# Performance work log

Measured on AMD Instinct MI355X. Metric: run time of the kernel, lower is better.

Reference implementation:

```python
import jax, jax.numpy as jnp
import numpy as np

N_NODES = 100000
N_EDGES = 500000
NODE_DIM = 32


def setup_inputs() -> dict:
    key = jax.random.key(0)
    k1, k2, k3, k4 = jax.random.split(key, 4)
    node_states = jax.random.normal(k1, (N_NODES, NODE_DIM), dtype=jnp.float32)
    edge_index = jax.random.randint(k2, (N_EDGES, 2), 0, N_NODES, dtype=jnp.int64)
    # Pre-encoded per-edge transform matrices (a_in), scaled like a learned encoder output
    a_in = jax.random.normal(k3, (N_EDGES, NODE_DIM, NODE_DIM), dtype=jnp.float32) / np.sqrt(NODE_DIM)
    bound = 1.0 / np.sqrt(NODE_DIM)
    bias = jax.random.uniform(k4, (NODE_DIM,), dtype=jnp.float32, minval=-bound, maxval=bound)
    return {"node_states": node_states, "edge_index": edge_index, "a_in": a_in, "bias": bias}


def reference(node_states, edge_index, a_in, bias):
    num_nodes, node_dim = node_states.shape
    src = edge_index[:, 0]  # message sender
    dst = edge_index[:, 1]  # message receiver
    # gather: [E, D]
    x_i = jnp.take(node_states, src, axis=0)
    # per-edge matmul: x_i[e] @ a_in[e] -> [E, D]
    msg = jnp.einsum('ed,edf->ef', x_i, a_in)
    # scatter-mean into node slots
    summed = jax.ops.segment_sum(msg, dst, num_segments=num_nodes)
    count = jax.ops.segment_sum(jnp.ones((msg.shape[0],), msg.dtype), dst, num_segments=num_nodes)
    mean = summed / jnp.maximum(count, 1.0)[:, None]
    return jax.nn.relu(mean + bias)
```

## Files before the change

kernel.cpp:

```cpp
#include <hip/hip_runtime.h>

#define NUM_NODES 100000
#define NODE_DIM 32

__global__ void mp_zero_kernel(float4* __restrict__ out4,
                               float4* __restrict__ cnt4,
                               int n_out4, int n_cnt4) {
    int t = blockIdx.x * blockDim.x + threadIdx.x;
    if (t < n_out4) {
        out4[t] = make_float4(0.f, 0.f, 0.f, 0.f);
    }
    int u = t - n_out4;
    if (u >= 0 && u < n_cnt4) {
        cnt4[u] = make_float4(0.f, 0.f, 0.f, 0.f);
    }
}

__global__ void mp_edge_kernel(const float* __restrict__ node_states,
                               const int* __restrict__ edge_index,
                               const float4* __restrict__ a4,
                               float* __restrict__ out_sum,
                               float* __restrict__ counts,
                               int n_edges) {
    int t = blockIdx.x * blockDim.x + threadIdx.x;
    int e = t >> 3;
    if (e >= n_edges) return;
    int j = t & 7;

    int src = edge_index[2 * e];
    int dst = edge_index[2 * e + 1];

    float4 x4 = reinterpret_cast<const float4*>(node_states)[src * 8 + j];
    float xs[4] = {x4.x, x4.y, x4.z, x4.w};

    const float4* A = a4 + (size_t)e * 256;
    float4 acc = make_float4(0.f, 0.f, 0.f, 0.f);

#pragma unroll
    for (int d = 0; d < 32; ++d) {
        float xd = __shfl(xs[d & 3], d >> 2, 8);
        float4 a = A[d * 8 + j];
        acc.x = fmaf(xd, a.x, acc.x);
        acc.y = fmaf(xd, a.y, acc.y);
        acc.z = fmaf(xd, a.z, acc.z);
        acc.w = fmaf(xd, a.w, acc.w);
    }

    float* o = out_sum + (size_t)dst * NODE_DIM + j * 4;
    atomicAdd(o + 0, acc.x);
    atomicAdd(o + 1, acc.y);
    atomicAdd(o + 2, acc.z);
    atomicAdd(o + 3, acc.w);
    if (j == 0) atomicAdd(counts + dst, 1.0f);
}

__global__ void mp_finalize_kernel(float4* __restrict__ out4,
                                   const float* __restrict__ counts,
                                   const float4* __restrict__ bias4,
                                   int n_nodes) {
    int t = blockIdx.x * blockDim.x + threadIdx.x;
    if (t >= n_nodes * 8) return;
    int n = t >> 3;
    int j = t & 7;
    float c = fmaxf(counts[n], 1.0f);
    float inv = 1.0f / c;
    float4 s = out4[t];
    float4 b = bias4[j];
    float4 r;
    r.x = fmaxf(fmaf(s.x, inv, b.x), 0.f);
    r.y = fmaxf(fmaf(s.y, inv, b.y), 0.f);
    r.z = fmaxf(fmaf(s.z, inv, b.z), 0.f);
    r.w = fmaxf(fmaf(s.w, inv, b.w), 0.f);
    out4[t] = r;
}

extern "C" void kernel_launch(void* const* d_in, const int* in_sizes, int n_in,
                              void* d_out, int out_size, void* d_ws, size_t ws_size,
                              hipStream_t stream) {
    const float* node_states = (const float*)d_in[0];
    const int*   edge_index  = (const int*)d_in[1];
    const float* a_in        = (const float*)d_in[2];
    const float* bias        = (const float*)d_in[3];

    int n_edges = in_sizes[1] / 2;
    int n_nodes = in_sizes[0] / NODE_DIM;

    float* out_sum = (float*)d_out;
    float* counts  = (float*)d_ws;

    int n_out4 = n_nodes * (NODE_DIM / 4);
    int n_cnt4 = (n_nodes + 3) / 4;
    {
        int total = n_out4 + n_cnt4;
        int blocks = (total + 255) / 256;
        mp_zero_kernel<<<blocks, 256, 0, stream>>>(
            (float4*)out_sum, (float4*)counts, n_out4, n_cnt4);
    }

    {
        long long total = (long long)n_edges * 8;
        int blocks = (int)((total + 255) / 256);
        mp_edge_kernel<<<blocks, 256, 0, stream>>>(
            node_states, edge_index, (const float4*)a_in,
            out_sum, counts, n_edges);
    }

    {
        int total = n_nodes * 8;
        int blocks = (total + 255) / 256;
        mp_finalize_kernel<<<blocks, 256, 0, stream>>>(
            (float4*)out_sum, counts, (const float4*)bias, n_nodes);
    }
}
```

Before: 433.9 us.

## Use persistent grid-stride edge loop with prefetch and nontemporal matrix loads

The edge kernel now runs a fixed grid of 2048 blocks that stride over edges. Each group of 8 threads prefetches the next edge's index pair and source node row while it processes the current edge. The per-edge matrix stream is read with nontemporal loads, so the 256 MB of one-use data does not evict reusable node and output lines from cache. Edge indices are loaded as one int2 instead of two scalar loads. The fixed grid size may underfill or over-serialize the device compared with one thread group per edge.

```diff
diff --git a/kernel.cpp b/kernel.cpp
--- a/kernel.cpp
+++ b/kernel.cpp
@@ -2,6 +2,8 @@
 
 #define NUM_NODES 100000
 #define NODE_DIM 32
+
+typedef float floatx4 __attribute__((ext_vector_type(4)));
 
 __global__ void mp_zero_kernel(float4* __restrict__ out4,
                                float4* __restrict__ cnt4,
@@ -18,40 +20,56 @@
 
 __global__ void mp_edge_kernel(const float* __restrict__ node_states,
                                const int* __restrict__ edge_index,
-                               const float4* __restrict__ a4,
+                               const floatx4* __restrict__ a4,
                                float* __restrict__ out_sum,
                                float* __restrict__ counts,
                                int n_edges) {
-    int t = blockIdx.x * blockDim.x + threadIdx.x;
-    int e = t >> 3;
+    int tid = blockIdx.x * blockDim.x + threadIdx.x;
+    int j = tid & 7;
+    int group = tid >> 3;
+    int ngroups = (gridDim.x * blockDim.x) >> 3;
+
+    int e = group;
     if (e >= n_edges) return;
-    int j = t & 7;
 
-    int src = edge_index[2 * e];
-    int dst = edge_index[2 * e + 1];
+    int2 ei = *reinterpret_cast<const int2*>(edge_index + 2 * (size_t)e);
+    float4 x4 = reinterpret_cast<const float4*>(node_states)[(size_t)ei.x * 8 + j];
 
-    float4 x4 = reinterpret_cast<const float4*>(node_states)[src * 8 + j];
-    float xs[4] = {x4.x, x4.y, x4.z, x4.w};
+    while (e < n_edges) {
+        int en = e + ngroups;
+        int2 ei_n;
+        float4 x4_n;
+        if (en < n_edges) {
+            ei_n = *reinterpret_cast<const int2*>(edge_index + 2 * (size_t)en);
+            x4_n = reinterpret_cast<const float4*>(node_states)[(size_t)ei_n.x * 8 + j];
+        }
 
-    const float4* A = a4 + (size_t)e * 256;
-    float4 acc = make_float4(0.f, 0.f, 0.f, 0.f);
+        float xs[4] = {x4.x, x4.y, x4.z, x4.w};
+        const floatx4* A = a4 + (size_t)e * 256;
+        float4 acc = make_float4(0.f, 0.f, 0.f, 0.f);
 
 #pragma unroll
-    for (int d = 0; d < 32; ++d) {
-        float xd = __shfl(xs[d & 3], d >> 2, 8);
-        float4 a = A[d * 8 + j];
-        acc.x = fmaf(xd, a.x, acc.x);
-        acc.y = fmaf(xd, a.y, acc.y);
-        acc.z = fmaf(xd, a.z, acc.z);
-        acc.w = fmaf(xd, a.w, acc.w);
+        for (int d = 0; d < 32; ++d) {
+            float xd = __shfl(xs[d & 3], d >> 2, 8);
+            floatx4 a = __builtin_nontemporal_load(&A[d * 8 + j]);
+            acc.x = fmaf(xd, a.x, acc.x);
+            acc.y = fmaf(xd, a.y, acc.y);
+            acc.z = fmaf(xd, a.z, acc.z);
+            acc.w = fmaf(xd, a.w, acc.w);
+        }
+
+        int dst = ei.y;
+        float* o = out_sum + (size_t)dst * NODE_DIM + j * 4;
+        atomicAdd(o + 0, acc.x);
+        atomicAdd(o + 1, acc.y);
+        atomicAdd(o + 2, acc.z);
+        atomicAdd(o + 3, acc.w);
+        if (j == 0) atomicAdd(counts + dst, 1.0f);
+
+        e = en;
+        ei = ei_n;
+        x4 = x4_n;
     }
-
-    float* o = out_sum + (size_t)dst * NODE_DIM + j * 4;
-    atomicAdd(o + 0, acc.x);
-    atomicAdd(o + 1, acc.y);
-    atomicAdd(o + 2, acc.z);
-    atomicAdd(o + 3, acc.w);
-    if (j == 0) atomicAdd(counts + dst, 1.0f);
 }
 
 __global__ void mp_finalize_kernel(float4* __restrict__ out4,
@@ -98,10 +116,9 @@
     }
 
     {
-        long long total = (long long)n_edges * 8;
-        int blocks = (int)((total + 255) / 256);
+        int blocks = 2048;
         mp_edge_kernel<<<blocks, 256, 0, stream>>>(
-            node_states, edge_index, (const float4*)a_in,
+            node_states, edge_index, (const floatx4*)a_in,
             out_sum, counts, n_edges);
     }
 
```

New measurement: 397.7 us. -8.3%, faster.
